# Kernel optimization log

Hardware: AMD Instinct MI355X
Metric: run time of the kernel (lower is better)

Reference implementation:

```python
import jax, jax.numpy as jnp
import numpy as np

N_NODES, N_EDGES, D = 50000, 640000, 128

def setup_inputs() -> dict:
    key = jax.random.key(0)
    ks = jax.random.split(key, 8)
    s = 0.05
    return {
        'node_h': jax.random.normal(ks[0], (N_NODES, D), jnp.float32),
        'edge_h': jax.random.normal(ks[1], (N_EDGES, D), jnp.float32),
        'src': jax.random.randint(ks[2], (N_EDGES,), 0, N_NODES, jnp.int32),
        'dst': jax.random.randint(ks[3], (N_EDGES,), 0, N_NODES, jnp.int32),
        'We1': jax.random.normal(ks[4], (3 * D, D), jnp.float32) * s,
        'be1': jnp.zeros((D,), jnp.float32),
        'We2': jax.random.normal(ks[5], (D, D), jnp.float32) * s,
        'be2': jnp.zeros((D,), jnp.float32),
        'Wn1': jax.random.normal(ks[6], (2 * D, D), jnp.float32) * s,
        'bn1': jnp.zeros((D,), jnp.float32),
        'Wn2': jax.random.normal(ks[7], (D, D), jnp.float32) * s,
        'bn2': jnp.zeros((D,), jnp.float32),
    }

def reference(node_h, edge_h, src, dst, We1, be1, We2, be2, Wn1, bn1, Wn2, bn2):
    # edge update: concat(src h, dst h, edge h) -> edge MLP  [E, 3D] -> [E, D]
    e_in = jnp.concatenate([node_h[src], node_h[dst], edge_h], axis=-1)
    e_new = jax.nn.relu(e_in @ We1 + be1) @ We2 + be2
    # message = copy_e('h'), reduce = sum -> segment_sum over destination nodes
    agg_m = jax.ops.segment_sum(e_new, dst, num_segments=node_h.shape[0])
    # node update: concat(agg_m, node h) -> node MLP  [N, 2D] -> [N, D]
    n_in = jnp.concatenate([agg_m, node_h], axis=-1)
    n_new = jax.nn.relu(n_in @ Wn1 + bn1) @ Wn2 + bn2
    return n_new
```

## Files before the change

### kernel.cpp

```cpp
#include <hip/hip_runtime.h>

#define NN 50000
#define NE 640000
#define DD 128

typedef float f32x4 __attribute__((ext_vector_type(4)));
typedef __bf16 bf16x8 __attribute__((ext_vector_type(8)));
typedef unsigned short u16x8 __attribute__((ext_vector_type(8)));

__device__ inline __bf16 f2bf(float f) {
  unsigned u = __builtin_bit_cast(unsigned, f);
  u = (u + 0x7fffu + ((u >> 16) & 1u)) >> 16;
  unsigned short h = (unsigned short)u;
  return __builtin_bit_cast(__bf16, h);
}
__device__ inline unsigned short f2bfu(float f) {
  return __builtin_bit_cast(unsigned short, f2bf(f));
}
__device__ inline float bf2f(unsigned bits16) {
  return __builtin_bit_cast(float, bits16 << 16);
}
__device__ inline float bfval(__bf16 h) {
  return bf2f((unsigned)__builtin_bit_cast(unsigned short, h));
}

__device__ inline bf16x8 load8(const float* __restrict__ p) {
  f32x4 a = *(const f32x4*)p;
  f32x4 b = *(const f32x4*)(p + 4);
  bf16x8 o;
  o[0] = f2bf(a[0]); o[1] = f2bf(a[1]); o[2] = f2bf(a[2]); o[3] = f2bf(a[3]);
  o[4] = f2bf(b[0]); o[5] = f2bf(b[1]); o[6] = f2bf(b[2]); o[7] = f2bf(b[3]);
  return o;
}

#define MFMA16(a, b, c) __builtin_amdgcn_mfma_f32_16x16x32_bf16((a), (b), (c), 0, 0, 0)

__global__ void prep_kernel(const float* __restrict__ We1, const float* __restrict__ We2,
                            const float* __restrict__ Wn1, const float* __restrict__ Wn2,
                            __bf16* __restrict__ We1t, __bf16* __restrict__ We2t,
                            __bf16* __restrict__ Wn1t, __bf16* __restrict__ Wn2t) {
  int i = blockIdx.x * blockDim.x + threadIdx.x;
  if (i < 49152) {
    int n = i / 384, k = i % 384;
    We1t[i] = f2bf(We1[k * 128 + n]);
  } else if (i < 65536) {
    int j = i - 49152; int n = j / 128, k = j % 128;
    We2t[j] = f2bf(We2[k * 128 + n]);
  } else if (i < 98304) {
    int j = i - 65536; int n = j / 256, k = j % 256;
    Wn1t[j] = f2bf(Wn1[k * 128 + n]);
  } else if (i < 114688) {
    int j = i - 98304; int n = j / 128, k = j % 128;
    Wn2t[j] = f2bf(Wn2[k * 128 + n]);
  }
}

__global__ void conv_node_kernel(const float* __restrict__ nh,
                                 unsigned short* __restrict__ nhb) {
  int i = blockIdx.x * 256 + threadIdx.x;
  if (i >= NN * DD / 8) return;
  const float* p = nh + (size_t)i * 8;
  f32x4 a = *(const f32x4*)p;
  f32x4 b = *(const f32x4*)(p + 4);
  u16x8 o;
  o[0] = f2bfu(a[0]); o[1] = f2bfu(a[1]); o[2] = f2bfu(a[2]); o[3] = f2bfu(a[3]);
  o[4] = f2bfu(b[0]); o[5] = f2bfu(b[1]); o[6] = f2bfu(b[2]); o[7] = f2bfu(b[3]);
  *(u16x8*)(nhb + (size_t)i * 8) = o;
}

__global__ __launch_bounds__(256) void dnode_kernel(
    const unsigned short* __restrict__ nhb, const __bf16* __restrict__ We1t,
    const float* __restrict__ be1, float* __restrict__ Dg) {
  const int tid = (int)threadIdx.x;
  const int w = tid >> 6;
  const int l = tid & 63;
  const int lm = l & 15;
  const int q = l >> 4;
  const int n0 = (int)blockIdx.x * 128;
  const int row0 = w * 32;

  int r0 = n0 + row0 + lm;
  int r1 = r0 + 16;
  int c0 = r0 < NN ? r0 : NN - 1;
  int c1 = r1 < NN ? r1 : NN - 1;

  f32x4 acc[2][8];
#pragma unroll
  for (int nt = 0; nt < 8; ++nt) {
    float b = be1[nt * 16 + lm];
    acc[0][nt] = (f32x4){b, b, b, b};
    acc[1][nt] = (f32x4){b, b, b, b};
  }
#pragma unroll
  for (int s = 0; s < 4; ++s) {
    const int col = s * 32 + q * 8;
    bf16x8 a0 = __builtin_bit_cast(bf16x8, *(const u16x8*)(nhb + (size_t)c0 * DD + col));
    bf16x8 a1 = __builtin_bit_cast(bf16x8, *(const u16x8*)(nhb + (size_t)c1 * DD + col));
    const __bf16* bp = We1t + (size_t)lm * 384 + 128 + s * 32 + q * 8;
#pragma unroll
    for (int nt = 0; nt < 8; ++nt) {
      bf16x8 bb = *(const bf16x8*)(bp + nt * 16 * 384);
      acc[0][nt] = MFMA16(a0, bb, acc[0][nt]);
      acc[1][nt] = MFMA16(a1, bb, acc[1][nt]);
    }
  }
#pragma unroll
  for (int t = 0; t < 2; ++t) {
#pragma unroll
    for (int r = 0; r < 4; ++r) {
      int node = n0 + row0 + t * 16 + q * 4 + r;
      if (node < NN) {
        float* orow = Dg + (size_t)node * DD + lm;
#pragma unroll
        for (int nt = 0; nt < 8; ++nt)
          orow[nt * 16] = acc[t][nt][r];
      }
    }
  }
}

__global__ void hist_kernel(const int* __restrict__ dst, int* __restrict__ counts) {
  int i = blockIdx.x * 256 + threadIdx.x;
  if (i < NE) atomicAdd(&counts[dst[i]], 1);
}
__global__ void scan1_kernel(const int* __restrict__ counts, int* __restrict__ basearr,
                             int* __restrict__ partials) {
  __shared__ int sd[256];
  int t = threadIdx.x;
  int i = blockIdx.x * 256 + t;
  int v = (i < NN) ? counts[i] : 0;
  sd[t] = v; __syncthreads();
  for (int off = 1; off < 256; off <<= 1) {
    int x = (t >= off) ? sd[t - off] : 0;
    __syncthreads();
    sd[t] += x;
    __syncthreads();
  }
  if (i < NN) basearr[i] = sd[t] - v;
  if (t == 255) partials[blockIdx.x] = sd[255];
}
__global__ void scan2_kernel(const int* __restrict__ partials, int* __restrict__ poff,
                             int nparts) {
  __shared__ int sd[256];
  int t = threadIdx.x;
  int v = (t < nparts) ? partials[t] : 0;
  sd[t] = v; __syncthreads();
  for (int off = 1; off < 256; off <<= 1) {
    int x = (t >= off) ? sd[t - off] : 0;
    __syncthreads();
    sd[t] += x;
    __syncthreads();
  }
  if (t < nparts) poff[t] = sd[t] - v;
}
__global__ void scatter_kernel(const int* __restrict__ src, const int* __restrict__ dst,
                               const int* __restrict__ basearr, const int* __restrict__ poff,
                               int* __restrict__ cursor, int* __restrict__ eids,
                               int* __restrict__ sidv, int* __restrict__ dstv) {
  int i = blockIdx.x * 256 + threadIdx.x;
  if (i < NE) {
    int d = dst[i];
    int p = basearr[d] + poff[d >> 8] + atomicAdd(&cursor[d], 1);
    eids[p] = i;
    sidv[p] = src[i];
    dstv[p] = d;
  }
}

__global__ __launch_bounds__(256) void edge_agg_kernel(
    const unsigned short* __restrict__ nhb, const float* __restrict__ edge_h,
    const int* __restrict__ eids, const int* __restrict__ sidv,
    const int* __restrict__ dstv, const float* __restrict__ Dg,
    const __bf16* __restrict__ We1t, float* __restrict__ S) {
  __shared__ unsigned short h1[128 * 136];
  __shared__ int dloc[128];
  __shared__ int sidx[128];
  __shared__ int segdst[128];
  __shared__ int wcnt0s, nsegS;
  float* Dlds = (float*)h1;

  const int tid = (int)threadIdx.x;
  const int w = tid >> 6;
  const int l = tid & 63;
  const int lm = l & 15;
  const int q = l >> 4;
  const int e0 = (int)blockIdx.x * 128;
  const int row0 = w * 32;
  const int p0 = e0 + row0 + lm;
  const int p1 = p0 + 16;

  const unsigned short* sp0 = nhb + (size_t)sidv[p0] * DD;
  const unsigned short* sp1 = nhb + (size_t)sidv[p1] * DD;
  const float* ehp0 = edge_h + (size_t)eids[p0] * DD;
  const float* ehp1 = edge_h + (size_t)eids[p1] * DD;

  u16x8 sa0[4], sa1[4];
#pragma unroll
  for (int s = 0; s < 4; ++s) {
    sa0[s] = *(const u16x8*)(sp0 + s * 32 + q * 8);
    sa1[s] = *(const u16x8*)(sp1 + s * 32 + q * 8);
  }
  bf16x8 ea0[4], ea1[4];
#pragma unroll
  for (int s = 0; s < 4; ++s) {
    ea0[s] = load8(ehp0 + s * 32 + q * 8);
    ea1[s] = load8(ehp1 + s * 32 + q * 8);
  }

  int d = 0, flag = 0, idx = 0;
  if (tid < 128) {
    d = dstv[e0 + tid];
    dloc[tid] = d;
    int dp = (tid == 0) ? -1 : dstv[e0 + tid - 1];
    flag = (d != dp) ? 1 : 0;
    unsigned long long mask = __ballot(flag);
    int lane = tid & 63;
    idx = (int)__popcll(mask & ((1ull << lane) - 1)) + flag - 1;
    if (tid == 63) wcnt0s = (int)__popcll(mask);
  }
  __syncthreads();
  if (tid < 128) {
    if (tid >= 64) idx += wcnt0s;
    sidx[tid] = idx;
    if (flag) segdst[idx] = d;
    if (tid == 127) nsegS = idx + 1;
  }
  __syncthreads();
  const int nsegT = nsegS;

  {
    const int nstage = nsegT < 64 ? nsegT : 64;
    const int total = nstage << 7;
    for (int base = 0; base < total; base += 1024) {
      float v[4];
#pragma unroll
      for (int u = 0; u < 4; ++u) {
        int i = base + u * 256 + tid;
        if (i < total) v[u] = Dg[(size_t)segdst[i >> 7] * DD + (i & 127)];
      }
#pragma unroll
      for (int u = 0; u < 4; ++u) {
        int i = base + u * 256 + tid;
        if (i < total) Dlds[(i >> 7) * 129 + (i & 127)] = v[u];
      }
    }
  }

  f32x4 acc[2][8];
#pragma unroll
  for (int nt = 0; nt < 8; ++nt) {
    acc[0][nt] = (f32x4){0.f, 0.f, 0.f, 0.f};
    acc[1][nt] = (f32x4){0.f, 0.f, 0.f, 0.f};
  }
#pragma unroll
  for (int s = 0; s < 4; ++s) {
    bf16x8 a0 = __builtin_bit_cast(bf16x8, sa0[s]);
    bf16x8 a1 = __builtin_bit_cast(bf16x8, sa1[s]);
    const __bf16* bp = We1t + (size_t)lm * 384 + s * 32 + q * 8;
#pragma unroll
    for (int nt = 0; nt < 8; ++nt) {
      bf16x8 bb = *(const bf16x8*)(bp + nt * 16 * 384);
      acc[0][nt] = MFMA16(a0, bb, acc[0][nt]);
      acc[1][nt] = MFMA16(a1, bb, acc[1][nt]);
    }
  }
#pragma unroll
  for (int s = 0; s < 4; ++s) {
    const __bf16* bp = We1t + (size_t)lm * 384 + 256 + s * 32 + q * 8;
#pragma unroll
    for (int nt = 0; nt < 8; ++nt) {
      bf16x8 bb = *(const bf16x8*)(bp + nt * 16 * 384);
      acc[0][nt] = MFMA16(ea0[s], bb, acc[0][nt]);
      acc[1][nt] = MFMA16(ea1[s], bb, acc[1][nt]);
    }
  }
  __syncthreads();

  if (nsegT <= 64) {
#pragma unroll
    for (int t = 0; t < 2; ++t)
#pragma unroll
      for (int r = 0; r < 4; ++r) {
        int row = row0 + t * 16 + q * 4 + r;
        int si = sidx[row];
#pragma unroll
        for (int nt = 0; nt < 8; ++nt) {
          float v = acc[t][nt][r] + Dlds[si * 129 + nt * 16 + lm];
          acc[t][nt][r] = v > 0.f ? v : 0.f;
        }
      }
  } else {
#pragma unroll
    for (int t = 0; t < 2; ++t)
#pragma unroll
      for (int r = 0; r < 4; ++r) {
        int row = row0 + t * 16 + q * 4 + r;
        const float* drow = Dg + (size_t)dloc[row] * DD + lm;
#pragma unroll
        for (int nt = 0; nt < 8; ++nt) {
          float v = acc[t][nt][r] + drow[nt * 16];
          acc[t][nt][r] = v > 0.f ? v : 0.f;
        }
      }
  }
  __syncthreads();

#pragma unroll
  for (int t = 0; t < 2; ++t)
#pragma unroll
    for (int nt = 0; nt < 8; ++nt)
#pragma unroll
      for (int r = 0; r < 4; ++r) {
        int m = row0 + t * 16 + q * 4 + r;
        h1[m * 136 + nt * 16 + lm] = f2bfu(acc[t][nt][r]);
      }
  __syncthreads();

  {
    const int col = tid & 127;
    const int rbeg = (tid >> 7) * 64;
    const int rend = rbeg + 64;
    float a = 0.f;
    int dcur = dloc[rbeg];
    for (int r = rbeg; r < rend; ++r) {
      int dd = dloc[r];
      if (dd != dcur) {
        unsafeAtomicAdd(&S[(size_t)dcur * DD + col], a);
        a = 0.f;
        dcur = dd;
      }
      a += bf2f((unsigned)h1[r * 136 + col]);
    }
    unsafeAtomicAdd(&S[(size_t)dcur * DD + col], a);
  }
}

__global__ __launch_bounds__(256) void node_kernel2(
    const unsigned short* __restrict__ nhb, const float* __restrict__ S,
    const int* __restrict__ counts,
    const __bf16* __restrict__ We2t, const float* __restrict__ be2,
    const __bf16* __restrict__ Wn1t, const float* __restrict__ bn1,
    const __bf16* __restrict__ Wn2t, const float* __restrict__ bn2,
    float* __restrict__ out) {
  __shared__ unsigned short h1[128 * 136];
  const int tid = (int)threadIdx.x;
  const int w = tid >> 6;
  const int l = tid & 63;
  const int lm = l & 15;
  const int q = l >> 4;
  const int n0 = (int)blockIdx.x * 128;
  const int row0 = w * 32;

  int r0 = n0 + row0 + lm;
  int r1 = r0 + 16;
  int c0 = r0 < NN ? r0 : NN - 1;
  int c1 = r1 < NN ? r1 : NN - 1;
  const float* s0p = S + (size_t)c0 * DD;
  const float* s1p = S + (size_t)c1 * DD;

  f32x4 acc[2][8];

  {
    float cnt0[4], cnt1[4];
#pragma unroll
    for (int r = 0; r < 4; ++r) {
      int ra = n0 + row0 + q * 4 + r;
      int rb = ra + 16;
      cnt0[r] = (ra < NN) ? (float)counts[ra] : 0.f;
      cnt1[r] = (rb < NN) ? (float)counts[rb] : 0.f;
    }
#pragma unroll
    for (int nt = 0; nt < 8; ++nt) {
      float b = be2[nt * 16 + lm];
#pragma unroll
      for (int r = 0; r < 4; ++r) {
        acc[0][nt][r] = cnt0[r] * b;
        acc[1][nt][r] = cnt1[r] * b;
      }
    }
  }
#pragma unroll
  for (int step = 0; step < 4; ++step) {
    const int col = step * 32 + q * 8;
    f32x4 x0a = *(const f32x4*)(s0p + col);
    f32x4 x0b = *(const f32x4*)(s0p + col + 4);
    f32x4 x1a = *(const f32x4*)(s1p + col);
    f32x4 x1b = *(const f32x4*)(s1p + col + 4);
    bf16x8 h0, l0, h8, l8;
#pragma unroll
    for (int j = 0; j < 4; ++j) {
      float v = x0a[j]; __bf16 hh = f2bf(v);
      h0[j] = hh; l0[j] = f2bf(v - bfval(hh));
      v = x0b[j]; hh = f2bf(v);
      h0[j + 4] = hh; l0[j + 4] = f2bf(v - bfval(hh));
      v = x1a[j]; hh = f2bf(v);
      h8[j] = hh; l8[j] = f2bf(v - bfval(hh));
      v = x1b[j]; hh = f2bf(v);
      h8[j + 4] = hh; l8[j + 4] = f2bf(v - bfval(hh));
    }
    const __bf16* bp = We2t + (size_t)lm * 128 + step * 32 + q * 8;
#pragma unroll
    for (int nt = 0; nt < 8; ++nt) {
      bf16x8 bb = *(const bf16x8*)(bp + nt * 16 * 128);
      acc[0][nt] = MFMA16(h0, bb, acc[0][nt]);
      acc[0][nt] = MFMA16(l0, bb, acc[0][nt]);
      acc[1][nt] = MFMA16(h8, bb, acc[1][nt]);
      acc[1][nt] = MFMA16(l8, bb, acc[1][nt]);
    }
  }

#pragma unroll
  for (int t = 0; t < 2; ++t)
#pragma unroll
    for (int nt = 0; nt < 8; ++nt)
#pragma unroll
      for (int r = 0; r < 4; ++r) {
        int m = row0 + t * 16 + q * 4 + r;
        h1[m * 136 + nt * 16 + lm] = f2bfu(acc[t][nt][r]);
      }
  __syncthreads();

#pragma unroll
  for (int nt = 0; nt < 8; ++nt) {
    float b = bn1[nt * 16 + lm];
    acc[0][nt] = (f32x4){b, b, b, b};
    acc[1][nt] = (f32x4){b, b, b, b};
  }
#pragma unroll
  for (int step = 0; step < 8; ++step) {
    bf16x8 a0, a1;
    if (step < 4) {
      a0 = __builtin_bit_cast(bf16x8, *(const u16x8*)&h1[(row0 + lm) * 136 + step * 32 + q * 8]);
      a1 = __builtin_bit_cast(bf16x8, *(const u16x8*)&h1[(row0 + 16 + lm) * 136 + step * 32 + q * 8]);
    } else {
      const int col = (step - 4) * 32 + q * 8;
      a0 = __builtin_bit_cast(bf16x8, *(const u16x8*)(nhb + (size_t)c0 * DD + col));
      a1 = __builtin_bit_cast(bf16x8, *(const u16x8*)(nhb + (size_t)c1 * DD + col));
    }
    const __bf16* bp = Wn1t + (size_t)lm * 256 + step * 32 + q * 8;
#pragma unroll
    for (int nt = 0; nt < 8; ++nt) {
      bf16x8 bb = *(const bf16x8*)(bp + nt * 16 * 256);
      acc[0][nt] = MFMA16(a0, bb, acc[0][nt]);
      acc[1][nt] = MFMA16(a1, bb, acc[1][nt]);
    }
  }
  __syncthreads();

#pragma unroll
  for (int t = 0; t < 2; ++t)
#pragma unroll
    for (int nt = 0; nt < 8; ++nt)
#pragma unroll
      for (int r = 0; r < 4; ++r) {
        float v = acc[t][nt][r];
        v = v > 0.f ? v : 0.f;
        int m = row0 + t * 16 + q * 4 + r;
        h1[m * 136 + nt * 16 + lm] = f2bfu(v);
      }
  __syncthreads();

#pragma unroll
  for (int nt = 0; nt < 8; ++nt) {
    float b = bn2[nt * 16 + lm];
    acc[0][nt] = (f32x4){b, b, b, b};
    acc[1][nt] = (f32x4){b, b, b, b};
  }
#pragma unroll
  for (int step = 0; step < 4; ++step) {
    bf16x8 a0 = __builtin_bit_cast(bf16x8, *(const u16x8*)&h1[(row0 + lm) * 136 + step * 32 + q * 8]);
    bf16x8 a1 = __builtin_bit_cast(bf16x8, *(const u16x8*)&h1[(row0 + 16 + lm) * 136 + step * 32 + q * 8]);
    const __bf16* bp = Wn2t + (size_t)lm * 128 + step * 32 + q * 8;
#pragma unroll
    for (int nt = 0; nt < 8; ++nt) {
      bf16x8 bb = *(const bf16x8*)(bp + nt * 16 * 128);
      acc[0][nt] = MFMA16(a0, bb, acc[0][nt]);
      acc[1][nt] = MFMA16(a1, bb, acc[1][nt]);
    }
  }

#pragma unroll
  for (int t = 0; t < 2; ++t) {
#pragma unroll
    for (int r = 0; r < 4; ++r) {
      int node = n0 + row0 + t * 16 + q * 4 + r;
      if (node < NN) {
        float* orow = out + (size_t)node * DD + lm;
#pragma unroll
        for (int nt = 0; nt < 8; ++nt)
          orow[nt * 16] = acc[t][nt][r];
      }
    }
  }
}

__global__ __launch_bounds__(256) void edge_fb_kernel(
    const float* __restrict__ node_h, const float* __restrict__ edge_h,
    const int* __restrict__ src, const int* __restrict__ dst,
    const __bf16* __restrict__ We1t, const float* __restrict__ be1,
    const __bf16* __restrict__ We2t, const float* __restrict__ be2,
    float* __restrict__ agg) {
  __shared__ unsigned short h1[128 * 136];
  const int tid = (int)threadIdx.x;
  const int w = tid >> 6;
  const int l = tid & 63;
  const int lm = l & 15;
  const int q = l >> 4;
  const int e0 = (int)blockIdx.x * 128;
  const int row0 = w * 32;

  const int eA0 = e0 + row0 + lm;
  const int eA1 = eA0 + 16;
  const float* srcA0[3];
  const float* srcA1[3];
  srcA0[0] = node_h + (size_t)src[eA0] * DD;
  srcA0[1] = node_h + (size_t)dst[eA0] * DD;
  srcA0[2] = edge_h + (size_t)eA0 * DD;
  srcA1[0] = node_h + (size_t)src[eA1] * DD;
  srcA1[1] = node_h + (size_t)dst[eA1] * DD;
  srcA1[2] = edge_h + (size_t)eA1 * DD;

  f32x4 acc[2][8];
#pragma unroll
  for (int nt = 0; nt < 8; ++nt) {
    float b = be1[nt * 16 + lm];
    acc[0][nt] = (f32x4){b, b, b, b};
    acc[1][nt] = (f32x4){b, b, b, b};
  }
#pragma unroll
  for (int step = 0; step < 12; ++step) {
    const int region = step >> 2;
    const int col = ((step & 3) * 32) + q * 8;
    bf16x8 a0 = load8(srcA0[region] + col);
    bf16x8 a1 = load8(srcA1[region] + col);
    const __bf16* bp = We1t + (size_t)lm * 384 + step * 32 + q * 8;
#pragma unroll
    for (int nt = 0; nt < 8; ++nt) {
      bf16x8 bb = *(const bf16x8*)(bp + nt * 16 * 384);
      acc[0][nt] = MFMA16(a0, bb, acc[0][nt]);
      acc[1][nt] = MFMA16(a1, bb, acc[1][nt]);
    }
  }
#pragma unroll
  for (int t = 0; t < 2; ++t)
#pragma unroll
    for (int nt = 0; nt < 8; ++nt)
#pragma unroll
      for (int r = 0; r < 4; ++r) {
        float v = acc[t][nt][r];
        v = v > 0.f ? v : 0.f;
        int m = row0 + t * 16 + q * 4 + r;
        h1[m * 136 + nt * 16 + lm] = f2bfu(v);
      }
  __syncthreads();
#pragma unroll
  for (int nt = 0; nt < 8; ++nt) {
    float b = be2[nt * 16 + lm];
    acc[0][nt] = (f32x4){b, b, b, b};
    acc[1][nt] = (f32x4){b, b, b, b};
  }
#pragma unroll
  for (int step = 0; step < 4; ++step) {
    bf16x8 a0 = __builtin_bit_cast(bf16x8, *(const u16x8*)&h1[(row0 + lm) * 136 + step * 32 + q * 8]);
    bf16x8 a1 = __builtin_bit_cast(bf16x8, *(const u16x8*)&h1[(row0 + 16 + lm) * 136 + step * 32 + q * 8]);
    const __bf16* bp = We2t + (size_t)lm * 128 + step * 32 + q * 8;
#pragma unroll
    for (int nt = 0; nt < 8; ++nt) {
      bf16x8 bb = *(const bf16x8*)(bp + nt * 16 * 128);
      acc[0][nt] = MFMA16(a0, bb, acc[0][nt]);
      acc[1][nt] = MFMA16(a1, bb, acc[1][nt]);
    }
  }
#pragma unroll
  for (int t = 0; t < 2; ++t) {
#pragma unroll
    for (int r = 0; r < 4; ++r) {
      int e = e0 + row0 + t * 16 + q * 4 + r;
      float* arow = agg + (size_t)dst[e] * DD + lm;
#pragma unroll
      for (int nt = 0; nt < 8; ++nt)
        unsafeAtomicAdd(arow + nt * 16, acc[t][nt][r]);
    }
  }
}

__global__ __launch_bounds__(256) void node_fb_kernel(
    const float* __restrict__ node_h, const float* __restrict__ agg,
    const __bf16* __restrict__ Wn1t, const float* __restrict__ bn1,
    const __bf16* __restrict__ Wn2t, const float* __restrict__ bn2,
    float* __restrict__ out) {
  __shared__ unsigned short h1[128 * 136];
  const int tid = (int)threadIdx.x;
  const int w = tid >> 6;
  const int l = tid & 63;
  const int lm = l & 15;
  const int q = l >> 4;
  const int n0 = (int)blockIdx.x * 128;
  const int row0 = w * 32;

  int r0 = n0 + row0 + lm;
  int r1 = r0 + 16;
  int c0 = r0 < NN ? r0 : NN - 1;
  int c1 = r1 < NN ? r1 : NN - 1;
  const float* srcA0[2] = {agg + (size_t)c0 * DD, node_h + (size_t)c0 * DD};
  const float* srcA1[2] = {agg + (size_t)c1 * DD, node_h + (size_t)c1 * DD};

  f32x4 acc[2][8];
#pragma unroll
  for (int nt = 0; nt < 8; ++nt) {
    float b = bn1[nt * 16 + lm];
    acc[0][nt] = (f32x4){b, b, b, b};
    acc[1][nt] = (f32x4){b, b, b, b};
  }
#pragma unroll
  for (int step = 0; step < 8; ++step) {
    const int region = step >> 2;
    const int col = ((step & 3) * 32) + q * 8;
    bf16x8 a0 = load8(srcA0[region] + col);
    bf16x8 a1 = load8(srcA1[region] + col);
    const __bf16* bp = Wn1t + (size_t)lm * 256 + step * 32 + q * 8;
#pragma unroll
    for (int nt = 0; nt < 8; ++nt) {
      bf16x8 bb = *(const bf16x8*)(bp + nt * 16 * 256);
      acc[0][nt] = MFMA16(a0, bb, acc[0][nt]);
      acc[1][nt] = MFMA16(a1, bb, acc[1][nt]);
    }
  }
#pragma unroll
  for (int t = 0; t < 2; ++t)
#pragma unroll
    for (int nt = 0; nt < 8; ++nt)
#pragma unroll
      for (int r = 0; r < 4; ++r) {
        float v = acc[t][nt][r];
        v = v > 0.f ? v : 0.f;
        int m = row0 + t * 16 + q * 4 + r;
        h1[m * 136 + nt * 16 + lm] = f2bfu(v);
      }
  __syncthreads();
#pragma unroll
  for (int nt = 0; nt < 8; ++nt) {
    float b = bn2[nt * 16 + lm];
    acc[0][nt] = (f32x4){b, b, b, b};
    acc[1][nt] = (f32x4){b, b, b, b};
  }
#pragma unroll
  for (int step = 0; step < 4; ++step) {
    bf16x8 a0 = __builtin_bit_cast(bf16x8, *(const u16x8*)&h1[(row0 + lm) * 136 + step * 32 + q * 8]);
    bf16x8 a1 = __builtin_bit_cast(bf16x8, *(const u16x8*)&h1[(row0 + 16 + lm) * 136 + step * 32 + q * 8]);
    const __bf16* bp = Wn2t + (size_t)lm * 128 + step * 32 + q * 8;
#pragma unroll
    for (int nt = 0; nt < 8; ++nt) {
      bf16x8 bb = *(const bf16x8*)(bp + nt * 16 * 128);
      acc[0][nt] = MFMA16(a0, bb, acc[0][nt]);
      acc[1][nt] = MFMA16(a1, bb, acc[1][nt]);
    }
  }
#pragma unroll
  for (int t = 0; t < 2; ++t) {
#pragma unroll
    for (int r = 0; r < 4; ++r) {
      int node = n0 + row0 + t * 16 + q * 4 + r;
      if (node < NN) {
        float* orow = out + (size_t)node * DD + lm;
#pragma unroll
        for (int nt = 0; nt < 8; ++nt)
          orow[nt * 16] = acc[t][nt][r];
      }
    }
  }
}

extern "C" void kernel_launch(void* const* d_in, const int* in_sizes, int n_in,
                              void* d_out, int out_size, void* d_ws, size_t ws_size,
                              hipStream_t stream) {
  const float* node_h = (const float*)d_in[0];
  const float* edge_h = (const float*)d_in[1];
  const int* src = (const int*)d_in[2];
  const int* dst = (const int*)d_in[3];
  const float* We1 = (const float*)d_in[4];
  const float* be1 = (const float*)d_in[5];
  const float* We2 = (const float*)d_in[6];
  const float* be2 = (const float*)d_in[7];
  const float* Wn1 = (const float*)d_in[8];
  const float* bn1 = (const float*)d_in[9];
  const float* Wn2 = (const float*)d_in[10];
  const float* bn2 = (const float*)d_in[11];

  const size_t o_S    = 0;
  const size_t o_D    = 25600000;
  const size_t o_nhb  = 51200000;
  const size_t o_we1  = 64000000;
  const size_t o_we2  = 64098304;
  const size_t o_wn1  = 64131072;
  const size_t o_wn2  = 64196608;
  const size_t o_cnt  = 64229376;
  const size_t o_base = 64429376;
  const size_t o_cur  = 64629376;
  const size_t o_poff = 64829376;
  const size_t o_eids = 64830400;
  const size_t o_sidv = 67390400;
  const size_t o_dstv = 69950400;
  const size_t csr_need = 72510400;

  char* ws = (char*)d_ws;

  if (ws_size >= csr_need) {
    float* S     = (float*)(ws + o_S);
    float* Dg    = (float*)(ws + o_D);
    unsigned short* nhb = (unsigned short*)(ws + o_nhb);
    __bf16* We1t = (__bf16*)(ws + o_we1);
    __bf16* We2t = (__bf16*)(ws + o_we2);
    __bf16* Wn1t = (__bf16*)(ws + o_wn1);
    __bf16* Wn2t = (__bf16*)(ws + o_wn2);
    int* counts  = (int*)(ws + o_cnt);
    int* basearr = (int*)(ws + o_base);
    int* cursor  = (int*)(ws + o_cur);
    int* poff    = (int*)(ws + o_poff);
    int* eids    = (int*)(ws + o_eids);
    int* sidv    = (int*)(ws + o_sidv);
    int* dstv    = (int*)(ws + o_dstv);

    hipMemsetAsync(S, 0, (size_t)NN * DD * sizeof(float), stream);
    hipMemsetAsync(counts, 0, NN * sizeof(int), stream);
    hipMemsetAsync(cursor, 0, NN * sizeof(int), stream);
    conv_node_kernel<<<(NN * DD / 8 + 255) / 256, 256, 0, stream>>>(node_h, nhb);
    prep_kernel<<<(114688 + 255) / 256, 256, 0, stream>>>(We1, We2, Wn1, Wn2,
                                                          We1t, We2t, Wn1t, Wn2t);
    dnode_kernel<<<(NN + 127) / 128, 256, 0, stream>>>(nhb, We1t, be1, Dg);
    hist_kernel<<<(NE + 255) / 256, 256, 0, stream>>>(dst, counts);
    const int nparts = (NN + 255) / 256;
    scan1_kernel<<<nparts, 256, 0, stream>>>(counts, basearr, cursor);
    scan2_kernel<<<1, 256, 0, stream>>>(cursor, poff, nparts);
    hipMemsetAsync(cursor, 0, NN * sizeof(int), stream);
    scatter_kernel<<<(NE + 255) / 256, 256, 0, stream>>>(src, dst, basearr, poff,
                                                         cursor, eids, sidv, dstv);
    edge_agg_kernel<<<NE / 128, 256, 0, stream>>>(nhb, edge_h, eids, sidv, dstv,
                                                  Dg, We1t, S);
    node_kernel2<<<(NN + 127) / 128, 256, 0, stream>>>(nhb, S, counts,
                                                       We2t, be2, Wn1t, bn1,
                                                       Wn2t, bn2, (float*)d_out);
  } else {
    const size_t agg_bytes = (size_t)NN * DD * sizeof(float);
    float* agg = (float*)d_ws;
    char* wbase = ws + agg_bytes;
    __bf16* We1t = (__bf16*)(wbase);
    __bf16* We2t = (__bf16*)(wbase + 98304);
    __bf16* Wn1t = (__bf16*)(wbase + 98304 + 32768);
    __bf16* Wn2t = (__bf16*)(wbase + 98304 + 32768 + 65536);

    hipMemsetAsync(agg, 0, agg_bytes, stream);
    prep_kernel<<<(114688 + 255) / 256, 256, 0, stream>>>(We1, We2, Wn1, Wn2,
                                                          We1t, We2t, Wn1t, Wn2t);
    edge_fb_kernel<<<NE / 128, 256, 0, stream>>>(node_h, edge_h, src, dst,
                                                 We1t, be1, We2t, be2, agg);
    node_fb_kernel<<<(NN + 127) / 128, 256, 0, stream>>>(node_h, agg, Wn1t, bn1,
                                                         Wn2t, bn2, (float*)d_out);
  }
}
```

Measured before the change: 841.6 us.

## Fuse setup kernels and memsets, stage We1 tiles in LDS for edge GEMM

Merges the node bf16 conversion, weight transpose, degree histogram and the zeroing of S and cursor into one multi-role launch, and merges scan1 with the Dnode GEMM, cutting several launches and memsets. In the edge aggregation kernel, the We1 slices for the edge and source features are now staged into swizzled LDS and read from there instead of being loaded straight from global memory. The edge-feature GEMM is issued before the source-node GEMM, and the Dg staging now happens after both GEMMs. This adds extra block barriers and per-block LDS staging traffic. Zeroing S inside a kernel may also be slower than the driver memset.

```diff
diff --git a/kernel.cpp b/kernel.cpp
--- a/kernel.cpp
+++ b/kernel.cpp
@@ -35,48 +35,89 @@
 
 #define MFMA16(a, b, c) __builtin_amdgcn_mfma_f32_16x16x32_bf16((a), (b), (c), 0, 0, 0)
 
-__global__ void prep_kernel(const float* __restrict__ We1, const float* __restrict__ We2,
-                            const float* __restrict__ Wn1, const float* __restrict__ Wn2,
-                            __bf16* __restrict__ We1t, __bf16* __restrict__ We2t,
-                            __bf16* __restrict__ Wn1t, __bf16* __restrict__ Wn2t) {
-  int i = blockIdx.x * blockDim.x + threadIdx.x;
-  if (i < 49152) {
-    int n = i / 384, k = i % 384;
-    We1t[i] = f2bf(We1[k * 128 + n]);
-  } else if (i < 65536) {
-    int j = i - 49152; int n = j / 128, k = j % 128;
-    We2t[j] = f2bf(We2[k * 128 + n]);
-  } else if (i < 98304) {
-    int j = i - 65536; int n = j / 256, k = j % 256;
-    Wn1t[j] = f2bf(Wn1[k * 128 + n]);
-  } else if (i < 114688) {
-    int j = i - 98304; int n = j / 128, k = j % 128;
-    Wn2t[j] = f2bf(Wn2[k * 128 + n]);
-  }
-}
-
-__global__ void conv_node_kernel(const float* __restrict__ nh,
-                                 unsigned short* __restrict__ nhb) {
-  int i = blockIdx.x * 256 + threadIdx.x;
-  if (i >= NN * DD / 8) return;
-  const float* p = nh + (size_t)i * 8;
-  f32x4 a = *(const f32x4*)p;
-  f32x4 b = *(const f32x4*)(p + 4);
-  u16x8 o;
-  o[0] = f2bfu(a[0]); o[1] = f2bfu(a[1]); o[2] = f2bfu(a[2]); o[3] = f2bfu(a[3]);
-  o[4] = f2bfu(b[0]); o[5] = f2bfu(b[1]); o[6] = f2bfu(b[2]); o[7] = f2bfu(b[3]);
-  *(u16x8*)(nhb + (size_t)i * 8) = o;
-}
-
-__global__ __launch_bounds__(256) void dnode_kernel(
+#define NB_CONV 3125
+#define NB_PREP 448
+#define NB_HIST 2500
+#define NB_SZ   1563
+#define NB_CZ   196
+__global__ __launch_bounds__(256) void setup_kernel(
+    const float* __restrict__ nh, unsigned short* __restrict__ nhb,
+    const float* __restrict__ We1, const float* __restrict__ We2,
+    const float* __restrict__ Wn1, const float* __restrict__ Wn2,
+    __bf16* __restrict__ We1t, __bf16* __restrict__ We2t,
+    __bf16* __restrict__ Wn1t, __bf16* __restrict__ Wn2t,
+    const int* __restrict__ dst, int* __restrict__ counts,
+    float* __restrict__ S, int* __restrict__ cursor) {
+  const int b = (int)blockIdx.x;
+  const int tid = (int)threadIdx.x;
+  if (b < NB_CONV) {
+    int i = b * 256 + tid;
+    const float* p = nh + (size_t)i * 8;
+    f32x4 a = *(const f32x4*)p;
+    f32x4 c = *(const f32x4*)(p + 4);
+    u16x8 o;
+    o[0] = f2bfu(a[0]); o[1] = f2bfu(a[1]); o[2] = f2bfu(a[2]); o[3] = f2bfu(a[3]);
+    o[4] = f2bfu(c[0]); o[5] = f2bfu(c[1]); o[6] = f2bfu(c[2]); o[7] = f2bfu(c[3]);
+    *(u16x8*)(nhb + (size_t)i * 8) = o;
+  } else if (b < NB_CONV + NB_PREP) {
+    int i = (b - NB_CONV) * 256 + tid;
+    if (i < 49152) {
+      int n = i / 384, k = i % 384;
+      We1t[i] = f2bf(We1[k * 128 + n]);
+    } else if (i < 65536) {
+      int j = i - 49152; int n = j / 128, k = j % 128;
+      We2t[j] = f2bf(We2[k * 128 + n]);
+    } else if (i < 98304) {
+      int j = i - 65536; int n = j / 256, k = j % 256;
+      Wn1t[j] = f2bf(Wn1[k * 128 + n]);
+    } else if (i < 114688) {
+      int j = i - 98304; int n = j / 128, k = j % 128;
+      Wn2t[j] = f2bf(Wn2[k * 128 + n]);
+    }
+  } else if (b < NB_CONV + NB_PREP + NB_HIST) {
+    int i = (b - NB_CONV - NB_PREP) * 256 + tid;
+    if (i < NE) atomicAdd(&counts[dst[i]], 1);
+  } else if (b < NB_CONV + NB_PREP + NB_HIST + NB_SZ) {
+    int fbase = (b - NB_CONV - NB_PREP - NB_HIST) * 4096 + tid * 16;
+    if (fbase + 16 <= NN * DD) {
+      f32x4 z = (f32x4){0.f, 0.f, 0.f, 0.f};
+      f32x4* p = (f32x4*)(S + fbase);
+      p[0] = z; p[1] = z; p[2] = z; p[3] = z;
+    }
+  } else {
+    int i = (b - NB_CONV - NB_PREP - NB_HIST - NB_SZ) * 256 + tid;
+    if (i < NN) cursor[i] = 0;
+  }
+}
+
+__global__ __launch_bounds__(256) void scan1_dnode_kernel(
+    const int* __restrict__ counts, int* __restrict__ basearr,
+    int* __restrict__ parts,
     const unsigned short* __restrict__ nhb, const __bf16* __restrict__ We1t,
     const float* __restrict__ be1, float* __restrict__ Dg) {
+  const int b = (int)blockIdx.x;
+  if (b < 196) {
+    __shared__ int sd[256];
+    int t = threadIdx.x;
+    int i = b * 256 + t;
+    int v = (i < NN) ? counts[i] : 0;
+    sd[t] = v; __syncthreads();
+    for (int off = 1; off < 256; off <<= 1) {
+      int x = (t >= off) ? sd[t - off] : 0;
+      __syncthreads();
+      sd[t] += x;
+      __syncthreads();
+    }
+    if (i < NN) basearr[i] = sd[t] - v;
+    if (t == 255) parts[b] = sd[255];
+    return;
+  }
   const int tid = (int)threadIdx.x;
   const int w = tid >> 6;
   const int l = tid & 63;
   const int lm = l & 15;
   const int q = l >> 4;
-  const int n0 = (int)blockIdx.x * 128;
+  const int n0 = (b - 196) * 128;
   const int row0 = w * 32;
 
   int r0 = n0 + row0 + lm;
@@ -87,9 +128,9 @@
   f32x4 acc[2][8];
 #pragma unroll
   for (int nt = 0; nt < 8; ++nt) {
-    float b = be1[nt * 16 + lm];
-    acc[0][nt] = (f32x4){b, b, b, b};
-    acc[1][nt] = (f32x4){b, b, b, b};
+    float bb = be1[nt * 16 + lm];
+    acc[0][nt] = (f32x4){bb, bb, bb, bb};
+    acc[1][nt] = (f32x4){bb, bb, bb, bb};
   }
 #pragma unroll
   for (int s = 0; s < 4; ++s) {
@@ -119,16 +160,11 @@
   }
 }
 
-__global__ void hist_kernel(const int* __restrict__ dst, int* __restrict__ counts) {
-  int i = blockIdx.x * 256 + threadIdx.x;
-  if (i < NE) atomicAdd(&counts[dst[i]], 1);
-}
-__global__ void scan1_kernel(const int* __restrict__ counts, int* __restrict__ basearr,
-                             int* __restrict__ partials) {
+__global__ void scan2_kernel(const int* __restrict__ parts, int* __restrict__ poff,
+                             int nparts) {
   __shared__ int sd[256];
   int t = threadIdx.x;
-  int i = blockIdx.x * 256 + t;
-  int v = (i < NN) ? counts[i] : 0;
+  int v = (t < nparts) ? parts[t] : 0;
   sd[t] = v; __syncthreads();
   for (int off = 1; off < 256; off <<= 1) {
     int x = (t >= off) ? sd[t - off] : 0;
@@ -136,23 +172,9 @@
     sd[t] += x;
     __syncthreads();
   }
-  if (i < NN) basearr[i] = sd[t] - v;
-  if (t == 255) partials[blockIdx.x] = sd[255];
-}
-__global__ void scan2_kernel(const int* __restrict__ partials, int* __restrict__ poff,
-                             int nparts) {
-  __shared__ int sd[256];
-  int t = threadIdx.x;
-  int v = (t < nparts) ? partials[t] : 0;
-  sd[t] = v; __syncthreads();
-  for (int off = 1; off < 256; off <<= 1) {
-    int x = (t >= off) ? sd[t - off] : 0;
-    __syncthreads();
-    sd[t] += x;
-    __syncthreads();
-  }
   if (t < nparts) poff[t] = sd[t] - v;
 }
+
 __global__ void scatter_kernel(const int* __restrict__ src, const int* __restrict__ dst,
                                const int* __restrict__ basearr, const int* __restrict__ poff,
                                int* __restrict__ cursor, int* __restrict__ eids,
@@ -167,17 +189,31 @@
   }
 }
 
+__device__ inline void stageB(unsigned short* lds16, const __bf16* __restrict__ We1t,
+                              int kbase, int tid) {
+  const int n = tid >> 1;
+  const int colb = (tid & 1) * 128;
+  const unsigned short* srcrow = (const unsigned short*)We1t + (size_t)n * 384 + kbase;
+  char* dstrow = (char*)lds16 + n * 256;
+  const int sw = (n & 15) << 4;
+#pragma unroll
+  for (int j = 0; j < 8; ++j) {
+    int cb = colb + j * 16;
+    u16x8 v = *(const u16x8*)(srcrow + cb / 2);
+    *(u16x8*)(dstrow + (cb ^ sw)) = v;
+  }
+}
+
 __global__ __launch_bounds__(256) void edge_agg_kernel(
     const unsigned short* __restrict__ nhb, const float* __restrict__ edge_h,
     const int* __restrict__ eids, const int* __restrict__ sidv,
     const int* __restrict__ dstv, const float* __restrict__ Dg,
     const __bf16* __restrict__ We1t, float* __restrict__ S) {
-  __shared__ unsigned short h1[128 * 136];
+  __shared__ unsigned short lds16[128 * 136];
   __shared__ int dloc[128];
   __shared__ int sidx[128];
   __shared__ int segdst[128];
   __shared__ int wcnt0s, nsegS;
-  float* Dlds = (float*)h1;
 
   const int tid = (int)threadIdx.x;
   const int w = tid >> 6;
@@ -189,22 +225,22 @@
   const int p0 = e0 + row0 + lm;
   const int p1 = p0 + 16;
 
+  const float* ehp0 = edge_h + (size_t)eids[p0] * DD;
+  const float* ehp1 = edge_h + (size_t)eids[p1] * DD;
   const unsigned short* sp0 = nhb + (size_t)sidv[p0] * DD;
   const unsigned short* sp1 = nhb + (size_t)sidv[p1] * DD;
-  const float* ehp0 = edge_h + (size_t)eids[p0] * DD;
-  const float* ehp1 = edge_h + (size_t)eids[p1] * DD;
-
+
+  bf16x8 ea0[4], ea1[4];
+#pragma unroll
+  for (int s = 0; s < 4; ++s) {
+    ea0[s] = load8(ehp0 + s * 32 + q * 8);
+    ea1[s] = load8(ehp1 + s * 32 + q * 8);
+  }
   u16x8 sa0[4], sa1[4];
 #pragma unroll
   for (int s = 0; s < 4; ++s) {
     sa0[s] = *(const u16x8*)(sp0 + s * 32 + q * 8);
     sa1[s] = *(const u16x8*)(sp1 + s * 32 + q * 8);
-  }
-  bf16x8 ea0[4], ea1[4];
-#pragma unroll
-  for (int s = 0; s < 4; ++s) {
-    ea0[s] = load8(ehp0 + s * 32 + q * 8);
-    ea1[s] = load8(ehp1 + s * 32 + q * 8);
   }
 
   int d = 0, flag = 0, idx = 0;
@@ -214,8 +250,7 @@
     int dp = (tid == 0) ? -1 : dstv[e0 + tid - 1];
     flag = (d != dp) ? 1 : 0;
     unsigned long long mask = __ballot(flag);
-    int lane = tid & 63;
-    idx = (int)__popcll(mask & ((1ull << lane) - 1)) + flag - 1;
+    idx = (int)__popcll(mask & ((1ull << (tid & 63)) - 1)) + flag - 1;
     if (tid == 63) wcnt0s = (int)__popcll(mask);
   }
   __syncthreads();
@@ -225,9 +260,46 @@
     if (flag) segdst[idx] = d;
     if (tid == 127) nsegS = idx + 1;
   }
-  __syncthreads();
+  stageB(lds16, We1t, 256, tid);
+  __syncthreads();
+
+  f32x4 acc[2][8];
+#pragma unroll
+  for (int nt = 0; nt < 8; ++nt) {
+    acc[0][nt] = (f32x4){0.f, 0.f, 0.f, 0.f};
+    acc[1][nt] = (f32x4){0.f, 0.f, 0.f, 0.f};
+  }
+  const char* Bb = (const char*)lds16;
+  const int swr = lm << 4;
+
+#pragma unroll
+  for (int s = 0; s < 4; ++s) {
+#pragma unroll
+    for (int nt = 0; nt < 8; ++nt) {
+      bf16x8 bb = *(const bf16x8*)(Bb + (nt * 16 + lm) * 256 + ((s * 64 + q * 16) ^ swr));
+      acc[0][nt] = MFMA16(ea0[s], bb, acc[0][nt]);
+      acc[1][nt] = MFMA16(ea1[s], bb, acc[1][nt]);
+    }
+  }
+  __syncthreads();
+  stageB(lds16, We1t, 0, tid);
+  __syncthreads();
+
+#pragma unroll
+  for (int s = 0; s < 4; ++s) {
+    bf16x8 a0 = __builtin_bit_cast(bf16x8, sa0[s]);
+    bf16x8 a1 = __builtin_bit_cast(bf16x8, sa1[s]);
+#pragma unroll
+    for (int nt = 0; nt < 8; ++nt) {
+      bf16x8 bb = *(const bf16x8*)(Bb + (nt * 16 + lm) * 256 + ((s * 64 + q * 16) ^ swr));
+      acc[0][nt] = MFMA16(a0, bb, acc[0][nt]);
+      acc[1][nt] = MFMA16(a1, bb, acc[1][nt]);
+    }
+  }
+  __syncthreads();
+
   const int nsegT = nsegS;
-
+  float* Dlds = (float*)lds16;
   {
     const int nstage = nsegT < 64 ? nsegT : 64;
     const int total = nstage << 7;
@@ -245,35 +317,6 @@
       }
     }
   }
-
-  f32x4 acc[2][8];
-#pragma unroll
-  for (int nt = 0; nt < 8; ++nt) {
-    acc[0][nt] = (f32x4){0.f, 0.f, 0.f, 0.f};
-    acc[1][nt] = (f32x4){0.f, 0.f, 0.f, 0.f};
-  }
-#pragma unroll
-  for (int s = 0; s < 4; ++s) {
-    bf16x8 a0 = __builtin_bit_cast(bf16x8, sa0[s]);
-    bf16x8 a1 = __builtin_bit_cast(bf16x8, sa1[s]);
-    const __bf16* bp = We1t + (size_t)lm * 384 + s * 32 + q * 8;
-#pragma unroll
-    for (int nt = 0; nt < 8; ++nt) {
-      bf16x8 bb = *(const bf16x8*)(bp + nt * 16 * 384);
-      acc[0][nt] = MFMA16(a0, bb, acc[0][nt]);
-      acc[1][nt] = MFMA16(a1, bb, acc[1][nt]);
-    }
-  }
-#pragma unroll
-  for (int s = 0; s < 4; ++s) {
-    const __bf16* bp = We1t + (size_t)lm * 384 + 256 + s * 32 + q * 8;
-#pragma unroll
-    for (int nt = 0; nt < 8; ++nt) {
-      bf16x8 bb = *(const bf16x8*)(bp + nt * 16 * 384);
-      acc[0][nt] = MFMA16(ea0[s], bb, acc[0][nt]);
-      acc[1][nt] = MFMA16(ea1[s], bb, acc[1][nt]);
-    }
-  }
   __syncthreads();
 
   if (nsegT <= 64) {
@@ -312,7 +355,7 @@
 #pragma unroll
       for (int r = 0; r < 4; ++r) {
         int m = row0 + t * 16 + q * 4 + r;
-        h1[m * 136 + nt * 16 + lm] = f2bfu(acc[t][nt][r]);
+        lds16[m * 136 + nt * 16 + lm] = f2bfu(acc[t][nt][r]);
       }
   __syncthreads();
 
@@ -329,7 +372,7 @@
         a = 0.f;
         dcur = dd;
       }
-      a += bf2f((unsigned)h1[r * 136 + col]);
+      a += bf2f((unsigned)lds16[r * 136 + col]);
     }
     unsafeAtomicAdd(&S[(size_t)dcur * DD + col], a);
   }
@@ -494,6 +537,26 @@
   }
 }
 
+__global__ void prep_fb_kernel(const float* __restrict__ We1, const float* __restrict__ We2,
+                               const float* __restrict__ Wn1, const float* __restrict__ Wn2,
+                               __bf16* __restrict__ We1t, __bf16* __restrict__ We2t,
+                               __bf16* __restrict__ Wn1t, __bf16* __restrict__ Wn2t) {
+  int i = blockIdx.x * blockDim.x + threadIdx.x;
+  if (i < 49152) {
+    int n = i / 384, k = i % 384;
+    We1t[i] = f2bf(We1[k * 128 + n]);
+  } else if (i < 65536) {
+    int j = i - 49152; int n = j / 128, k = j % 128;
+    We2t[j] = f2bf(We2[k * 128 + n]);
+  } else if (i < 98304) {
+    int j = i - 65536; int n = j / 256, k = j % 256;
+    Wn1t[j] = f2bf(Wn1[k * 128 + n]);
+  } else if (i < 114688) {
+    int j = i - 98304; int n = j / 128, k = j % 128;
+    Wn2t[j] = f2bf(Wn2[k * 128 + n]);
+  }
+}
+
 __global__ __launch_bounds__(256) void edge_fb_kernel(
     const float* __restrict__ node_h, const float* __restrict__ edge_h,
     const int* __restrict__ src, const int* __restrict__ dst,
@@ -701,7 +764,8 @@
   const size_t o_eids = 64830400;
   const size_t o_sidv = 67390400;
   const size_t o_dstv = 69950400;
-  const size_t csr_need = 72510400;
+  const size_t o_part = 72510400;
+  const size_t csr_need = 72511424;
 
   char* ws = (char*)d_ws;
 
@@ -720,19 +784,16 @@
     int* eids    = (int*)(ws + o_eids);
     int* sidv    = (int*)(ws + o_sidv);
     int* dstv    = (int*)(ws + o_dstv);
-
-    hipMemsetAsync(S, 0, (size_t)NN * DD * sizeof(float), stream);
+    int* parts   = (int*)(ws + o_part);
+
     hipMemsetAsync(counts, 0, NN * sizeof(int), stream);
-    hipMemsetAsync(cursor, 0, NN * sizeof(int), stream);
-    conv_node_kernel<<<(NN * DD / 8 + 255) / 256, 256, 0, stream>>>(node_h, nhb);
-    prep_kernel<<<(114688 + 255) / 256, 256, 0, stream>>>(We1, We2, Wn1, Wn2,
-                                                          We1t, We2t, Wn1t, Wn2t);
-    dnode_kernel<<<(NN + 127) / 128, 256, 0, stream>>>(nhb, We1t, be1, Dg);
-    hist_kernel<<<(NE + 255) / 256, 256, 0, stream>>>(dst, counts);
-    const int nparts = (NN + 255) / 256;
-    scan1_kernel<<<nparts, 256, 0, stream>>>(counts, basearr, cursor);
-    scan2_kernel<<<1, 256, 0, stream>>>(cursor, poff, nparts);
-    hipMemsetAsync(cursor, 0, NN * sizeof(int), stream);
+    const int nb_setup = NB_CONV + NB_PREP + NB_HIST + NB_SZ + NB_CZ;
+    setup_kernel<<<nb_setup, 256, 0, stream>>>(node_h, nhb, We1, We2, Wn1, Wn2,
+                                               We1t, We2t, Wn1t, Wn2t,
+                                               dst, counts, S, cursor);
+    scan1_dnode_kernel<<<196 + 391, 256, 0, stream>>>(counts, basearr, parts,
+                                                      nhb, We1t, be1, Dg);
+    scan2_kernel<<<1, 256, 0, stream>>>(parts, poff, 196);
     scatter_kernel<<<(NE + 255) / 256, 256, 0, stream>>>(src, dst, basearr, poff,
                                                          cursor, eids, sidv, dstv);
     edge_agg_kernel<<<NE / 128, 256, 0, stream>>>(nhb, edge_h, eids, sidv, dstv,
@@ -750,8 +811,8 @@
     __bf16* Wn2t = (__bf16*)(wbase + 98304 + 32768 + 65536);
 
     hipMemsetAsync(agg, 0, agg_bytes, stream);
-    prep_kernel<<<(114688 + 255) / 256, 256, 0, stream>>>(We1, We2, Wn1, Wn2,
-                                                          We1t, We2t, Wn1t, Wn2t);
+    prep_fb_kernel<<<(114688 + 255) / 256, 256, 0, stream>>>(We1, We2, Wn1, Wn2,
+                                                             We1t, We2t, Wn1t, Wn2t);
     edge_fb_kernel<<<NE / 128, 256, 0, stream>>>(node_h, edge_h, src, dst,
                                                  We1t, be1, We2t, be2, agg);
     node_fb_kernel<<<(NN + 127) / 128, 256, 0, stream>>>(node_h, agg, Wn1t, bn1,
```

After: 743.2 us. 11.7% less time.
